# Kernel tuning notes

Hardware: AMD Instinct MI355X
Metric: run time of the kernel (lower is better)

The kernel has to match this reference:

```python
import jax, jax.numpy as jnp
import numpy as np

RES = 96
MAX_X = 1.0
DX = np.float32(MAX_X / (RES / 2 - 1))


def _grid():
    # torch.linspace(dx*(1-res/2), dx*(res/2-1), res), meshgrid indexing='xy'
    x = jnp.linspace(DX * (1 - RES / 2), DX * (RES / 2 - 1), RES, dtype=jnp.float32)
    X, Y, Z = jnp.meshgrid(x, x, x, indexing='xy')
    return X, Y, Z


def _one_spatial_deriv(f):
    # torch.gradient(edge_order=1) == numpy/jnp.gradient default:
    # 2nd-order central interior, 1st-order one-sided edges.
    # Derivative index appended last, matching the module's einsum reorder.
    return jnp.stack([jnp.gradient(f, DX, axis=a) for a in range(3)], axis=-1)


def setup_inputs() -> dict:
    key = jax.random.key(0)
    k1, k2 = jax.random.split(key)
    BH_positions = jax.random.uniform(k1, (2, 3), dtype=jnp.float32, minval=-0.4, maxval=0.4)
    BH_masses_presoftplus = jax.random.uniform(k2, (2,), dtype=jnp.float32)
    return {"BH_positions": BH_positions, "BH_masses_presoftplus": BH_masses_presoftplus}


def reference(BH_positions, BH_masses_presoftplus):
    X, Y, Z = _grid()
    masses = jax.nn.softplus(BH_masses_presoftplus)  # [n]

    # BrillLindquist_init: psi = 1 + sum_n m_n / (2 r_n)
    dX = X[None] - BH_positions[:, 0, None, None, None]
    dY = Y[None] - BH_positions[:, 1, None, None, None]
    dZ = Z[None] - BH_positions[:, 2, None, None, None]
    r = jnp.sqrt(dX * dX + dY * dY + dZ * dZ)          # [n, res, res, res]
    psi = 1.0 + jnp.sum(masses[:, None, None, None] / (2.0 * r), axis=0)
    phi = jnp.log(psi)                                  # [res, res, res]

    eye = jnp.eye(3, dtype=phi.dtype)
    # gamma_bar_lo = I, gamma_bar_up = inv(I) = I
    gamma_mat_lo = jnp.exp(4.0 * phi)[..., None, None] * eye   # e^{4phi} gamma_bar_lo
    gamma_mat_up = jnp.exp(-4.0 * phi)[..., None, None] * eye  # e^{-4phi} gamma_bar_up

    # Christoffel symbols Gamma^i_{jk}
    dg = _one_spatial_deriv(gamma_mat_lo)  # [res,res,res,3,3,3], dg[...,a,b,c] = d_c gamma_{ab}
    s1 = jnp.einsum('xyzil,xyzjlk->xyzijk', gamma_mat_up, dg)
    s2 = jnp.einsum('xyzil,xyzlkj->xyzijk', gamma_mat_up, dg)
    s3 = jnp.einsum('xyzil,xyzjkl->xyzijk', gamma_mat_up, dg)
    Gamma_mat_up = 0.5 * (s1 + s2 - s3)    # [res,res,res,3,3,3]
    return Gamma_mat_up
```

## Files before the change

kernel.cpp:

```cpp
#include <hip/hip_runtime.h>
#include <math.h>

#define RES 96
#define NPTS (RES * RES * RES)
#define BLK  256
#define NBLK (NPTS / BLK)

struct BH {
    float bx0, by0, bz0, bx1, by1, bz1, hm0, hm1;
};

__device__ __forceinline__ float lin_coord(int t) {
    const float DXc   = 1.0f / 47.0f;
    const float start = -47.0f * DXc;
    const float stop  =  47.0f * DXc;
    const float step  = (stop - start) / 95.0f;
    return fmaf((float)t, step, start);
}

__device__ __forceinline__ float psi4_at(int a0, int a1, int a2, const BH& b) {
    float cx = lin_coord(a1);
    float cy = lin_coord(a0);
    float cz = lin_coord(a2);
    float dx0 = cx - b.bx0, dy0 = cy - b.by0, dz0 = cz - b.bz0;
    float dx1 = cx - b.bx1, dy1 = cy - b.by1, dz1 = cz - b.bz1;
    float r0 = sqrtf(dx0 * dx0 + dy0 * dy0 + dz0 * dz0);
    float r1 = sqrtf(dx1 * dx1 + dy1 * dy1 + dz1 * dz1);
    float psi = 1.0f + b.hm0 / r0 + b.hm1 / r1;
    float p2 = psi * psi;
    return p2 * p2;
}

__global__ __launch_bounds__(BLK) void gamma_kernel(
        const float* __restrict__ bh_pos,
        const float* __restrict__ bh_mpre,
        float* __restrict__ out)
{
    __shared__ float Gs[BLK * 3];
    const int tid = threadIdx.x;
    const int p   = blockIdx.x * BLK + tid;
    int a2 = p % RES;
    int t  = p / RES;
    int a1 = t % RES;
    int a0 = t / RES;

    BH b;
    b.bx0 = bh_pos[0]; b.by0 = bh_pos[1]; b.bz0 = bh_pos[2];
    b.bx1 = bh_pos[3]; b.by1 = bh_pos[4]; b.bz1 = bh_pos[5];
    b.hm0 = 0.5f * log1pf(expf(bh_mpre[0]));
    b.hm1 = 0.5f * log1pf(expf(bh_mpre[1]));

    const float DXc = 1.0f / 47.0f;
    float fc = psi4_at(a0, a1, a2, b);

    int a0m = a0 > 0 ? a0 - 1 : 0, a0p = a0 < RES - 1 ? a0 + 1 : RES - 1;
    int a1m = a1 > 0 ? a1 - 1 : 0, a1p = a1 < RES - 1 ? a1 + 1 : RES - 1;
    int a2m = a2 > 0 ? a2 - 1 : 0, a2p = a2 < RES - 1 ? a2 + 1 : RES - 1;

    float D0 = (psi4_at(a0p, a1, a2, b) - psi4_at(a0m, a1, a2, b)) / ((float)(a0p - a0m) * DXc);
    float D1 = (psi4_at(a0, a1p, a2, b) - psi4_at(a0, a1m, a2, b)) / ((float)(a1p - a1m) * DXc);
    float D2 = (psi4_at(a0, a1, a2p, b) - psi4_at(a0, a1, a2m, b)) / ((float)(a2p - a2m) * DXc);

    float E = 0.5f / fc;
    Gs[tid * 3 + 0] = E * D0;
    Gs[tid * 3 + 1] = E * D1;
    Gs[tid * 3 + 2] = E * D2;
    __syncthreads();

    float* oblk = out + (size_t)blockIdx.x * (BLK * 27);
#pragma unroll
    for (int w = 0; w < 27; ++w) {
        int e  = w * BLK + tid;
        int pl = e / 27;
        int c  = e - pl * 27;
        int i  = c / 9;
        int r  = c - 9 * i;
        int j  = r / 3;
        int k  = r - 3 * j;
        float v = 0.0f;
        if (i == j) v += Gs[pl * 3 + k];
        if (i == k) v += Gs[pl * 3 + j];
        if (j == k) v -= Gs[pl * 3 + i];
        oblk[e] = v;
    }
}

extern "C" void kernel_launch(void* const* d_in, const int* in_sizes, int n_in,
                              void* d_out, int out_size, void* d_ws, size_t ws_size,
                              hipStream_t stream) {
    const float* bh_pos  = (const float*)d_in[0];
    const float* bh_mpre = (const float*)d_in[1];
    float* out = (float*)d_out;
    gamma_kernel<<<NBLK, BLK, 0, stream>>>(bh_pos, bh_mpre, out);
}
```

Measured before the change: 127.2 us.

## Stage full 27-component tensor in LDS and store with float4 writes

Each thread now builds its own 27 Christoffel components in a 27KB shared buffer. The block then copies that buffer to global memory using coalesced float4 stores, where before it did 27 scalar stores with integer div/mod index decoding. The change also swaps sqrt/divide for hardware rsq/rcp intrinsics and replaces the derivative divide with a constant multiply. Costs are more LDS per block (lower occupancy possible), bank conflicts on the stride-27 per-thread writes, and slightly reduced precision from the approximate rsq/rcp.

```diff
diff --git a/kernel.cpp b/kernel.cpp
--- a/kernel.cpp
+++ b/kernel.cpp
@@ -5,6 +5,7 @@
 #define NPTS (RES * RES * RES)
 #define BLK  256
 #define NBLK (NPTS / BLK)
+#define F4_PER_BLK (BLK * 27 / 4)
 
 struct BH {
     float bx0, by0, bz0, bx1, by1, bz1, hm0, hm1;
@@ -24,9 +25,10 @@
     float cz = lin_coord(a2);
     float dx0 = cx - b.bx0, dy0 = cy - b.by0, dz0 = cz - b.bz0;
     float dx1 = cx - b.bx1, dy1 = cy - b.by1, dz1 = cz - b.bz1;
-    float r0 = sqrtf(dx0 * dx0 + dy0 * dy0 + dz0 * dz0);
-    float r1 = sqrtf(dx1 * dx1 + dy1 * dy1 + dz1 * dz1);
-    float psi = 1.0f + b.hm0 / r0 + b.hm1 / r1;
+    float dd0 = fmaf(dx0, dx0, fmaf(dy0, dy0, dz0 * dz0));
+    float dd1 = fmaf(dx1, dx1, fmaf(dy1, dy1, dz1 * dz1));
+    float psi = 1.0f + fmaf(b.hm0, __builtin_amdgcn_rsqf(dd0),
+                            b.hm1 * __builtin_amdgcn_rsqf(dd1));
     float p2 = psi * psi;
     return p2 * p2;
 }
@@ -36,7 +38,7 @@
         const float* __restrict__ bh_mpre,
         float* __restrict__ out)
 {
-    __shared__ float Gs[BLK * 3];
+    __shared__ __align__(16) float Gs27[BLK * 27];
     const int tid = threadIdx.x;
     const int p   = blockIdx.x * BLK + tid;
     int a2 = p % RES;
@@ -50,38 +52,41 @@
     b.hm0 = 0.5f * log1pf(expf(bh_mpre[0]));
     b.hm1 = 0.5f * log1pf(expf(bh_mpre[1]));
 
-    const float DXc = 1.0f / 47.0f;
     float fc = psi4_at(a0, a1, a2, b);
 
     int a0m = a0 > 0 ? a0 - 1 : 0, a0p = a0 < RES - 1 ? a0 + 1 : RES - 1;
     int a1m = a1 > 0 ? a1 - 1 : 0, a1p = a1 < RES - 1 ? a1 + 1 : RES - 1;
     int a2m = a2 > 0 ? a2 - 1 : 0, a2p = a2 < RES - 1 ? a2 + 1 : RES - 1;
+    float s0 = (a0p - a0m == 2) ? 23.5f : 47.0f;
+    float s1 = (a1p - a1m == 2) ? 23.5f : 47.0f;
+    float s2 = (a2p - a2m == 2) ? 23.5f : 47.0f;
 
-    float D0 = (psi4_at(a0p, a1, a2, b) - psi4_at(a0m, a1, a2, b)) / ((float)(a0p - a0m) * DXc);
-    float D1 = (psi4_at(a0, a1p, a2, b) - psi4_at(a0, a1m, a2, b)) / ((float)(a1p - a1m) * DXc);
-    float D2 = (psi4_at(a0, a1, a2p, b) - psi4_at(a0, a1, a2m, b)) / ((float)(a2p - a2m) * DXc);
+    float D0 = (psi4_at(a0p, a1, a2, b) - psi4_at(a0m, a1, a2, b)) * s0;
+    float D1 = (psi4_at(a0, a1p, a2, b) - psi4_at(a0, a1m, a2, b)) * s1;
+    float D2 = (psi4_at(a0, a1, a2p, b) - psi4_at(a0, a1, a2m, b)) * s2;
 
-    float E = 0.5f / fc;
-    Gs[tid * 3 + 0] = E * D0;
-    Gs[tid * 3 + 1] = E * D1;
-    Gs[tid * 3 + 2] = E * D2;
+    float E = 0.5f * __builtin_amdgcn_rcpf(fc);
+    float G0 = E * D0, G1 = E * D1, G2 = E * D2;
+
+    float G[3] = {G0, G1, G2};
+    float* myg = Gs27 + tid * 27;
+#pragma unroll
+    for (int c = 0; c < 27; ++c) {
+        const int i = c / 9, j = (c / 3) % 3, k = c % 3;
+        float v = 0.0f;
+        if (i == j) v += G[k];
+        if (i == k) v += G[j];
+        if (j == k) v -= G[i];
+        myg[c] = v;
+    }
     __syncthreads();
 
-    float* oblk = out + (size_t)blockIdx.x * (BLK * 27);
+    const float4* src = (const float4*)Gs27;
+    float4* dst = (float4*)(out + (size_t)blockIdx.x * (BLK * 27));
 #pragma unroll
-    for (int w = 0; w < 27; ++w) {
-        int e  = w * BLK + tid;
-        int pl = e / 27;
-        int c  = e - pl * 27;
-        int i  = c / 9;
-        int r  = c - 9 * i;
-        int j  = r / 3;
-        int k  = r - 3 * j;
-        float v = 0.0f;
-        if (i == j) v += Gs[pl * 3 + k];
-        if (i == k) v += Gs[pl * 3 + j];
-        if (j == k) v -= Gs[pl * 3 + i];
-        oblk[e] = v;
+    for (int w = 0; w < 7; ++w) {
+        int q = w * BLK + tid;
+        if (q < F4_PER_BLK) dst[q] = src[q];
     }
 }
 
```

New measurement: 103.5 us. 1.23x faster.
